# Kernel tuning notes

Measured on AMD Instinct MI355X. Metric: run time of the kernel, lower is better.

Reference implementation:

```python
import jax, jax.numpy as jnp
import numpy as np

QB = 64  # quantize_size from the source


def _blockwise_quant(y):
    """y: (N, R, C) softmax output. Quantize in 64x64 tiles to int8.
    Returns (q_int8 [N*g1*g2, QB*QB], s, z) matching the torch code."""
    N, R, C = y.shape
    g1, g2 = R // QB, C // QB
    # (N, g1, QB, g2, QB) -> (N, g1, g2, QB, QB) -> (N*g1*g2, QB*QB)
    b = y.reshape(N, g1, QB, g2, QB).transpose(0, 1, 3, 2, 4).reshape(-1, QB * QB)
    mx = jnp.max(b, axis=-1, keepdims=True)
    mn = jnp.min(b, axis=-1, keepdims=True)
    s = (mx - mn) / 255.0
    z = -mn / (s + 1e-10) - 128.0
    q = jnp.round(jnp.clip(b / (s + 1e-10) + z, -128.0, 127.0)).astype(jnp.int8)
    return q, s, z


def reference(x):
    # Forward: plain softmax over dim=-1; the int8 blockwise quantization is the
    # activation saved for backward (returned here so the workload isn't DCE'd).
    out = jax.nn.softmax(x, axis=-1)
    y = out.reshape(-1, x.shape[-2], x.shape[-1])
    q, s, z = _blockwise_quant(y)
    return out, q, s, z


def setup_inputs():
    key = jax.random.key(0)
    x = jax.random.normal(key, (2, 16, 2048, 2048), dtype=jnp.float32)
    return {"x": x}
```

## Files before the change

### kernel.cpp

```cpp
#include <hip/hip_runtime.h>
#include <math.h>


static constexpr int  COLS      = 2048;
static constexpr long long OUT_ELEMS = 134217728LL;
static constexpr int  NROWS     = 65536;
static constexpr int  NBLK      = 32768;

using v4f = __attribute__((ext_vector_type(4))) float;

__global__ __launch_bounds__(256) void rowstats_kernel(
    const float* __restrict__ x, float* __restrict__ stats)
{
    const int lane = threadIdx.x & 63;
    const int wave = threadIdx.x >> 6;
    const long long row = (long long)blockIdx.x * 4 + wave;
    const float* rp = x + row * COLS;

    float4 v[8];
#pragma unroll
    for (int c = 0; c < 8; ++c)
        v[c] = *reinterpret_cast<const float4*>(rp + c * 256 + lane * 4);

    float m = -INFINITY;
#pragma unroll
    for (int c = 0; c < 8; ++c)
        m = fmaxf(m, fmaxf(fmaxf(v[c].x, v[c].y), fmaxf(v[c].z, v[c].w)));
#pragma unroll
    for (int off = 32; off >= 1; off >>= 1)
        m = fmaxf(m, __shfl_xor(m, off, 64));

    float s = 0.0f;
#pragma unroll
    for (int c = 0; c < 8; ++c)
        s += __expf(v[c].x - m) + __expf(v[c].y - m) +
             __expf(v[c].z - m) + __expf(v[c].w - m);
#pragma unroll
    for (int off = 32; off >= 1; off >>= 1)
        s += __shfl_xor(s, off, 64);

    if (lane == 0) {
        stats[row * 2 + 0] = m;
        stats[row * 2 + 1] = 1.0f / s;
    }
}

__global__ __launch_bounds__(256) void panel_kernel(
    const float* __restrict__ x, const float* __restrict__ stats,
    float* __restrict__ out, float* __restrict__ qout,
    float* __restrict__ sout, float* __restrict__ zout)
{
    const int b  = 8191 - blockIdx.x;
    const int n  = b >> 8;
    const int i  = (b >> 3) & 31;
    const int jg = b & 7;
    const int t  = threadIdx.x;
    const int w  = t >> 6;
    const int l  = t & 63;

    const long long xbase = (long long)n * (COLS * (long long)COLS)
                          + (long long)(i * 64) * COLS + jg * 256;
    const int growbase = (n << 11) + i * 64;

    float4 p[16];
    float mn = INFINITY, mx = -INFINITY;
#pragma unroll
    for (int k = 0; k < 16; ++k) {
        const int r = (k << 2) + w;
        const float2 st = *reinterpret_cast<const float2*>(
            stats + (long long)(growbase + r) * 2);
        const v4f v = __builtin_nontemporal_load(
            (const v4f*)(x + xbase + (long long)r * COLS + l * 4));
        float4 pv;
        pv.x = __expf(v.x - st.x) * st.y;
        pv.y = __expf(v.y - st.x) * st.y;
        pv.z = __expf(v.z - st.x) * st.y;
        pv.w = __expf(v.w - st.x) * st.y;
        p[k] = pv;
        mn = fminf(mn, fminf(fminf(pv.x, pv.y), fminf(pv.z, pv.w)));
        mx = fmaxf(mx, fmaxf(fmaxf(pv.x, pv.y), fmaxf(pv.z, pv.w)));
    }
#pragma unroll
    for (int off = 8; off >= 1; off >>= 1) {
        mn = fminf(mn, __shfl_xor(mn, off, 64));
        mx = fmaxf(mx, __shfl_xor(mx, off, 64));
    }

    __shared__ float  smn[4][4], smx[4][4];
    __shared__ float2 sbc[4];
    if ((l & 15) == 0) { smn[w][l >> 4] = mn; smx[w][l >> 4] = mx; }
    __syncthreads();
    if (t < 4) {
        const float bmn = fminf(fminf(smn[0][t], smn[1][t]),
                                fminf(smn[2][t], smn[3][t]));
        const float bmx = fmaxf(fmaxf(smx[0][t], smx[1][t]),
                                fmaxf(smx[2][t], smx[3][t]));
        const float sc = (bmx - bmn) / 255.0f;
        const float d  = sc + 1e-10f;
        const float zz = -bmn / d - 128.0f;
        const int b4 = (n << 10) + (i << 5) + (jg << 2) + t;
        sout[b4] = sc;
        zout[b4] = zz;
        sbc[t] = make_float2(zz, 1.0f / d);
    }
    __syncthreads();

    const int   tl  = l >> 4;
    const float2 bc = sbc[tl];
    float* __restrict__ qb = qout
        + (long long)((n << 10) + (i << 5) + (jg << 2)) * 4096
        + tl * 4096 + (l & 15) * 4;

#pragma unroll
    for (int k = 0; k < 16; ++k) {
        const int r = (k << 2) + w;
        const float4 pv = p[k];
        __builtin_nontemporal_store(*(const v4f*)&pv,
            (v4f*)(out + xbase + (long long)r * COLS + l * 4));
        float4 qv;
        qv.x = roundf(fminf(fmaxf(pv.x * bc.y + bc.x, -128.0f), 127.0f));
        qv.y = roundf(fminf(fmaxf(pv.y * bc.y + bc.x, -128.0f), 127.0f));
        qv.z = roundf(fminf(fmaxf(pv.z * bc.y + bc.x, -128.0f), 127.0f));
        qv.w = roundf(fminf(fmaxf(pv.w * bc.y + bc.x, -128.0f), 127.0f));
        __builtin_nontemporal_store(*(const v4f*)&qv, (v4f*)(qb + r * 64));
    }
}

extern "C" void kernel_launch(void* const* d_in, const int* in_sizes, int n_in,
                              void* d_out, int out_size, void* d_ws, size_t ws_size,
                              hipStream_t stream) {
    const float* x = (const float*)d_in[0];
    float* out  = (float*)d_out;
    float* qout = out + OUT_ELEMS;
    float* sout = qout + OUT_ELEMS;
    float* zout = sout + NBLK;
    float* stats = (float*)d_ws;

    rowstats_kernel<<<NROWS / 4, 256, 0, stream>>>(x, stats);
    panel_kernel<<<8192, 256, 0, stream>>>(x, stats, out, qout, sout, zout);
}
```

Before: 353.0 us.

## Fuse row-stats and panel softmax-quant kernels into one row-panel kernel

Replaces the separate row-statistics pass and panel pass with a single kernel where each 1024-thread block handles a 64-row panel. It computes row max and sum into shared memory, then re-reads the panel (hopefully from cache) to produce softmax, per-tile min/max, and the quantized output. This removes the workspace stats round trip and aims to turn the second full read of x into a cache hit. The trade-off is large blocks with one barrier and lower occupancy per CU.

```diff
diff --git a/kernel.cpp b/kernel.cpp
--- a/kernel.cpp
+++ b/kernel.cpp
@@ -4,125 +4,108 @@
 
 static constexpr int  COLS      = 2048;
 static constexpr long long OUT_ELEMS = 134217728LL;
-static constexpr int  NROWS     = 65536;
 static constexpr int  NBLK      = 32768;
 
 using v4f = __attribute__((ext_vector_type(4))) float;
 
-__global__ __launch_bounds__(256) void rowstats_kernel(
-    const float* __restrict__ x, float* __restrict__ stats)
-{
-    const int lane = threadIdx.x & 63;
-    const int wave = threadIdx.x >> 6;
-    const long long row = (long long)blockIdx.x * 4 + wave;
-    const float* rp = x + row * COLS;
-
-    float4 v[8];
-#pragma unroll
-    for (int c = 0; c < 8; ++c)
-        v[c] = *reinterpret_cast<const float4*>(rp + c * 256 + lane * 4);
-
-    float m = -INFINITY;
-#pragma unroll
-    for (int c = 0; c < 8; ++c)
-        m = fmaxf(m, fmaxf(fmaxf(v[c].x, v[c].y), fmaxf(v[c].z, v[c].w)));
-#pragma unroll
-    for (int off = 32; off >= 1; off >>= 1)
-        m = fmaxf(m, __shfl_xor(m, off, 64));
-
-    float s = 0.0f;
-#pragma unroll
-    for (int c = 0; c < 8; ++c)
-        s += __expf(v[c].x - m) + __expf(v[c].y - m) +
-             __expf(v[c].z - m) + __expf(v[c].w - m);
-#pragma unroll
-    for (int off = 32; off >= 1; off >>= 1)
-        s += __shfl_xor(s, off, 64);
-
-    if (lane == 0) {
-        stats[row * 2 + 0] = m;
-        stats[row * 2 + 1] = 1.0f / s;
-    }
-}
-
-__global__ __launch_bounds__(256) void panel_kernel(
-    const float* __restrict__ x, const float* __restrict__ stats,
+__global__ __launch_bounds__(1024) void fused_kernel(
+    const float* __restrict__ x,
     float* __restrict__ out, float* __restrict__ qout,
     float* __restrict__ sout, float* __restrict__ zout)
 {
-    const int b  = 8191 - blockIdx.x;
-    const int n  = b >> 8;
-    const int i  = (b >> 3) & 31;
-    const int jg = b & 7;
-    const int t  = threadIdx.x;
-    const int w  = t >> 6;
-    const int l  = t & 63;
+    const int b = blockIdx.x;
+    const int n = b >> 5;
+    const int i = b & 31;
+    const int t = threadIdx.x;
+    const int w = t >> 6;
+    const int l = t & 63;
 
     const long long xbase = (long long)n * (COLS * (long long)COLS)
-                          + (long long)(i * 64) * COLS + jg * 256;
-    const int growbase = (n << 11) + i * 64;
+                          + (long long)(i * 64) * COLS;
 
-    float4 p[16];
-    float mn = INFINITY, mx = -INFINITY;
+    __shared__ float2 sst[64];
+
 #pragma unroll
-    for (int k = 0; k < 16; ++k) {
-        const int r = (k << 2) + w;
-        const float2 st = *reinterpret_cast<const float2*>(
-            stats + (long long)(growbase + r) * 2);
-        const v4f v = __builtin_nontemporal_load(
-            (const v4f*)(x + xbase + (long long)r * COLS + l * 4));
-        float4 pv;
-        pv.x = __expf(v.x - st.x) * st.y;
-        pv.y = __expf(v.y - st.x) * st.y;
-        pv.z = __expf(v.z - st.x) * st.y;
-        pv.w = __expf(v.w - st.x) * st.y;
-        p[k] = pv;
-        mn = fminf(mn, fminf(fminf(pv.x, pv.y), fminf(pv.z, pv.w)));
-        mx = fmaxf(mx, fmaxf(fmaxf(pv.x, pv.y), fmaxf(pv.z, pv.w)));
-    }
+    for (int rr = 0; rr < 4; ++rr) {
+        const int r = w + rr * 16;
+        const float* rp = x + xbase + (long long)r * COLS;
+        float4 v[8];
 #pragma unroll
-    for (int off = 8; off >= 1; off >>= 1) {
-        mn = fminf(mn, __shfl_xor(mn, off, 64));
-        mx = fmaxf(mx, __shfl_xor(mx, off, 64));
-    }
+        for (int c = 0; c < 8; ++c)
+            v[c] = *reinterpret_cast<const float4*>(rp + c * 256 + l * 4);
 
-    __shared__ float  smn[4][4], smx[4][4];
-    __shared__ float2 sbc[4];
-    if ((l & 15) == 0) { smn[w][l >> 4] = mn; smx[w][l >> 4] = mx; }
-    __syncthreads();
-    if (t < 4) {
-        const float bmn = fminf(fminf(smn[0][t], smn[1][t]),
-                                fminf(smn[2][t], smn[3][t]));
-        const float bmx = fmaxf(fmaxf(smx[0][t], smx[1][t]),
-                                fmaxf(smx[2][t], smx[3][t]));
-        const float sc = (bmx - bmn) / 255.0f;
-        const float d  = sc + 1e-10f;
-        const float zz = -bmn / d - 128.0f;
-        const int b4 = (n << 10) + (i << 5) + (jg << 2) + t;
-        sout[b4] = sc;
-        zout[b4] = zz;
-        sbc[t] = make_float2(zz, 1.0f / d);
+        float m = -INFINITY;
+#pragma unroll
+        for (int c = 0; c < 8; ++c)
+            m = fmaxf(m, fmaxf(fmaxf(v[c].x, v[c].y), fmaxf(v[c].z, v[c].w)));
+#pragma unroll
+        for (int off = 32; off >= 1; off >>= 1)
+            m = fmaxf(m, __shfl_xor(m, off, 64));
+
+        float s = 0.0f;
+#pragma unroll
+        for (int c = 0; c < 8; ++c)
+            s += __expf(v[c].x - m) + __expf(v[c].y - m) +
+                 __expf(v[c].z - m) + __expf(v[c].w - m);
+#pragma unroll
+        for (int off = 32; off >= 1; off >>= 1)
+            s += __shfl_xor(s, off, 64);
+
+        if (l == 0) sst[r] = make_float2(m, 1.0f / s);
     }
     __syncthreads();
 
-    const int   tl  = l >> 4;
-    const float2 bc = sbc[tl];
-    float* __restrict__ qb = qout
-        + (long long)((n << 10) + (i << 5) + (jg << 2)) * 4096
-        + tl * 4096 + (l & 15) * 4;
+#pragma unroll
+    for (int jj = 0; jj < 2; ++jj) {
+        const int j = w + jj * 16;
+        const long long tbase = xbase + j * 64;
+        const int cl = (l & 15) * 4;
+        const int rl = l >> 4;
 
+        float4 p[16];
+        float mn = INFINITY, mx = -INFINITY;
 #pragma unroll
-    for (int k = 0; k < 16; ++k) {
-        const int r = (k << 2) + w;
-        const float4 pv = p[k];
-        __builtin_nontemporal_store(*(const v4f*)&pv,
-            (v4f*)(out + xbase + (long long)r * COLS + l * 4));
-        float4 qv;
-        qv.x = roundf(fminf(fmaxf(pv.x * bc.y + bc.x, -128.0f), 127.0f));
-        qv.y = roundf(fminf(fmaxf(pv.y * bc.y + bc.x, -128.0f), 127.0f));
-        qv.z = roundf(fminf(fmaxf(pv.z * bc.y + bc.x, -128.0f), 127.0f));
-        qv.w = roundf(fminf(fmaxf(pv.w * bc.y + bc.x, -128.0f), 127.0f));
-        __builtin_nontemporal_store(*(const v4f*)&qv, (v4f*)(qb + r * 64));
+        for (int k = 0; k < 16; ++k) {
+            const int r = rl + 4 * k;
+            const float2 st = sst[r];
+            const float4 v = *reinterpret_cast<const float4*>(
+                x + tbase + (long long)r * COLS + cl);
+            float4 pv;
+            pv.x = __expf(v.x - st.x) * st.y;
+            pv.y = __expf(v.y - st.x) * st.y;
+            pv.z = __expf(v.z - st.x) * st.y;
+            pv.w = __expf(v.w - st.x) * st.y;
+            p[k] = pv;
+            mn = fminf(mn, fminf(fminf(pv.x, pv.y), fminf(pv.z, pv.w)));
+            mx = fmaxf(mx, fmaxf(fmaxf(pv.x, pv.y), fmaxf(pv.z, pv.w)));
+        }
+#pragma unroll
+        for (int off = 32; off >= 1; off >>= 1) {
+            mn = fminf(mn, __shfl_xor(mn, off, 64));
+            mx = fmaxf(mx, __shfl_xor(mx, off, 64));
+        }
+
+        const float sc  = (mx - mn) / 255.0f;
+        const float d   = sc + 1e-10f;
+        const float zz  = -mn / d - 128.0f;
+        const float rcp = 1.0f / d;
+        const int b4 = (n << 10) + (i << 5) + j;
+        if (l == 0) { sout[b4] = sc; zout[b4] = zz; }
+
+        float* __restrict__ qb = qout + (long long)b4 * 4096 + cl;
+#pragma unroll
+        for (int k = 0; k < 16; ++k) {
+            const int r = rl + 4 * k;
+            const float4 pv = p[k];
+            __builtin_nontemporal_store(*(const v4f*)&pv,
+                (v4f*)(out + tbase + (long long)r * COLS + cl));
+            float4 qv;
+            qv.x = roundf(fminf(fmaxf(pv.x * rcp + zz, -128.0f), 127.0f));
+            qv.y = roundf(fminf(fmaxf(pv.y * rcp + zz, -128.0f), 127.0f));
+            qv.z = roundf(fminf(fmaxf(pv.z * rcp + zz, -128.0f), 127.0f));
+            qv.w = roundf(fminf(fmaxf(pv.w * rcp + zz, -128.0f), 127.0f));
+            __builtin_nontemporal_store(*(const v4f*)&qv, (v4f*)(qb + r * 64));
+        }
     }
 }
 
@@ -134,8 +117,6 @@
     float* qout = out + OUT_ELEMS;
     float* sout = qout + OUT_ELEMS;
     float* zout = sout + NBLK;
-    float* stats = (float*)d_ws;
 
-    rowstats_kernel<<<NROWS / 4, 256, 0, stream>>>(x, stats);
-    panel_kernel<<<8192, 256, 0, stream>>>(x, stats, out, qout, sout, zout);
+    fused_kernel<<<1024, 1024, 0, stream>>>(x, out, qout, sout, zout);
 }
```

Measured after the change: 416.2 us. 17.9% more time.
